# Optimization experiments

Hardware: AMD Instinct MI355X
Metric: run time of the kernel (lower is better)

The kernel has to match this reference:

```python
import jax, jax.numpy as jnp
import numpy as np

EMB = 1024
FF = 1024
EPS = 1e-5

def _layernorm(x, g, b):
    mu = jnp.mean(x, axis=-1, keepdims=True)
    var = jnp.mean((x - mu) ** 2, axis=-1, keepdims=True)
    return (x - mu) * jax.lax.rsqrt(var + EPS) * g + b

def setup_inputs() -> dict:
    key = jax.random.key(0)
    ks = jax.random.split(key, 12)
    s = 1.0 / np.sqrt(EMB)
    x = jax.random.normal(ks[0], (4, 2048, EMB), dtype=jnp.float32)
    Wq = jax.random.normal(ks[1], (EMB, EMB), dtype=jnp.float32) * s
    bq = jnp.zeros((EMB,), jnp.float32)
    Wk = jax.random.normal(ks[2], (EMB, EMB), dtype=jnp.float32) * s
    bk = jnp.zeros((EMB,), jnp.float32)
    Wv = jax.random.normal(ks[3], (EMB, EMB), dtype=jnp.float32) * s
    bv = jnp.zeros((EMB,), jnp.float32)
    Wo = jax.random.normal(ks[4], (EMB, EMB), dtype=jnp.float32) * s
    bo = jnp.zeros((EMB,), jnp.float32)
    W1 = jax.random.normal(ks[5], (EMB, FF), dtype=jnp.float32) * s
    b1 = jnp.zeros((FF,), jnp.float32)
    W2 = jax.random.normal(ks[6], (FF, EMB), dtype=jnp.float32) * (1.0 / np.sqrt(FF))
    b2 = jnp.zeros((EMB,), jnp.float32)
    g1 = jnp.ones((EMB,), jnp.float32); be1 = jnp.zeros((EMB,), jnp.float32)
    g2 = jnp.ones((EMB,), jnp.float32); be2 = jnp.zeros((EMB,), jnp.float32)
    return {"x": x, "Wq": Wq, "bq": bq, "Wk": Wk, "bk": bk, "Wv": Wv, "bv": bv,
            "Wo": Wo, "bo": bo, "W1": W1, "b1": b1, "W2": W2, "b2": b2,
            "g1": g1, "be1": be1, "g2": g2, "be2": be2}

def reference(x, Wq, bq, Wk, bk, Wv, bv, Wo, bo, W1, b1, W2, b2, g1, be1, g2, be2):
    # pre-norm single-head self-attention + residual + FFN (dropout = identity, eval)
    xn = _layernorm(x, g1, be1)
    q = xn @ Wq + bq
    k = xn @ Wk + bk
    v = xn @ Wv + bv
    scores = jnp.einsum('bse,bte->bst', q, k) / jnp.sqrt(jnp.float32(EMB))
    w = jax.nn.softmax(scores, axis=-1)              # [B,S,S]
    attn = jnp.einsum('bst,bte->bse', w, v) @ Wo + bo
    x2 = x + attn
    xn2 = _layernorm(x2, g2, be2)
    ff = jax.nn.relu(xn2 @ W1 + b1) @ W2 + b2
    out = x2 + ff
    return (out, w)
```

## Files before the change

### kernel.cpp

```cpp
#include <hip/hip_runtime.h>

typedef __attribute__((ext_vector_type(8))) __bf16 bf16x8;
typedef __attribute__((ext_vector_type(4))) float f32x4;
typedef __attribute__((ext_vector_type(8))) ushort ushort8;

#define GLP(p) ((const __attribute__((address_space(1))) void*)(p))
#define LDP(p) ((__attribute__((address_space(3))) void*)(p))

__device__ __forceinline__ ushort f2b(float f) {
  union { float f; uint u; } c; c.f = f;
  uint u = c.u;
  uint r = (u + 0x7fffu + ((u >> 16) & 1u)) >> 16;
  return (ushort)r;
}

__device__ __forceinline__ float block_reduce_sum(float v, float* sm) {
#pragma unroll
  for (int off = 1; off < 64; off <<= 1) v += __shfl_xor(v, off);
  const int wave = threadIdx.x >> 6, lane = threadIdx.x & 63;
  __syncthreads();
  if (lane == 0) sm[wave] = v;
  __syncthreads();
  return sm[0] + sm[1] + sm[2] + sm[3];
}

__global__ __launch_bounds__(256) void wtrans6_kernel(
    const float* __restrict__ W0, const float* __restrict__ W1,
    const float* __restrict__ W2, const float* __restrict__ W3,
    const float* __restrict__ W4, const float* __restrict__ W5,
    ushort* __restrict__ T0, ushort* __restrict__ T1, ushort* __restrict__ T2,
    ushort* __restrict__ T3, ushort* __restrict__ T4, ushort* __restrict__ T5) {
  __shared__ float tile[32][33];
  const float* Ws[6] = {W0, W1, W2, W3, W4, W5};
  ushort* Ts[6] = {T0, T1, T2, T3, T4, T5};
  const float* W = Ws[blockIdx.z];
  ushort* Wt = Ts[blockIdx.z];
  const int K = 1024, N = 1024;
  const int n0 = blockIdx.x * 32, k0 = blockIdx.y * 32;
  const int tx = threadIdx.x, ty = threadIdx.y;
#pragma unroll
  for (int i = 0; i < 32; i += 8)
    tile[ty + i][tx] = W[(long)(k0 + ty + i) * N + n0 + tx];
  __syncthreads();
#pragma unroll
  for (int i = 0; i < 32; i += 8)
    Wt[(long)(n0 + ty + i) * K + k0 + tx] = f2b(tile[tx][ty + i]);
}

__global__ __launch_bounds__(256) void layernorm_kernel(
    const float* __restrict__ x, const float* __restrict__ g,
    const float* __restrict__ be, ushort* __restrict__ out) {
  __shared__ float sm[4];
  const long row = blockIdx.x;
  const float4 v = reinterpret_cast<const float4*>(x + row * 1024)[threadIdx.x];
  float s = v.x + v.y + v.z + v.w;
  s = block_reduce_sum(s, sm);
  const float mu = s * (1.0f / 1024.0f);
  const float dx = v.x - mu, dy = v.y - mu, dz = v.z - mu, dw = v.w - mu;
  float s2 = dx * dx + dy * dy + dz * dz + dw * dw;
  s2 = block_reduce_sum(s2, sm);
  const float rstd = rsqrtf(s2 * (1.0f / 1024.0f) + 1e-5f);
  const float4 gg = reinterpret_cast<const float4*>(g)[threadIdx.x];
  const float4 bb = reinterpret_cast<const float4*>(be)[threadIdx.x];
  ushort4 o;
  o.x = f2b(dx * rstd * gg.x + bb.x);
  o.y = f2b(dy * rstd * gg.y + bb.y);
  o.z = f2b(dz * rstd * gg.z + bb.z);
  o.w = f2b(dw * rstd * gg.w + bb.w);
  reinterpret_cast<ushort4*>(out + row * 1024)[threadIdx.x] = o;
}

__global__ __launch_bounds__(256) void softmax_kernel(
    float* __restrict__ s, ushort* __restrict__ wb) {
  __shared__ float sm[4];
  const long row = blockIdx.x;
  float4* r4 = reinterpret_cast<float4*>(s + row * 2048);
  float4 v0 = r4[threadIdx.x * 2];
  float4 v1 = r4[threadIdx.x * 2 + 1];
  float m = fmaxf(fmaxf(fmaxf(v0.x, v0.y), fmaxf(v0.z, v0.w)),
                  fmaxf(fmaxf(v1.x, v1.y), fmaxf(v1.z, v1.w)));
#pragma unroll
  for (int off = 1; off < 64; off <<= 1) m = fmaxf(m, __shfl_xor(m, off));
  const int wave = threadIdx.x >> 6, lane = threadIdx.x & 63;
  if (lane == 0) sm[wave] = m;
  __syncthreads();
  m = fmaxf(fmaxf(sm[0], sm[1]), fmaxf(sm[2], sm[3]));
  v0.x = expf(v0.x - m); v0.y = expf(v0.y - m);
  v0.z = expf(v0.z - m); v0.w = expf(v0.w - m);
  v1.x = expf(v1.x - m); v1.y = expf(v1.y - m);
  v1.z = expf(v1.z - m); v1.w = expf(v1.w - m);
  float sum = v0.x + v0.y + v0.z + v0.w + v1.x + v1.y + v1.z + v1.w;
  sum = block_reduce_sum(sum, sm);
  const float inv = 1.0f / sum;
  v0.x *= inv; v0.y *= inv; v0.z *= inv; v0.w *= inv;
  v1.x *= inv; v1.y *= inv; v1.z *= inv; v1.w *= inv;
  r4[threadIdx.x * 2] = v0;
  r4[threadIdx.x * 2 + 1] = v1;
  ushort8 o;
  o[0] = f2b(v0.x); o[1] = f2b(v0.y); o[2] = f2b(v0.z); o[3] = f2b(v0.w);
  o[4] = f2b(v1.x); o[5] = f2b(v1.y); o[6] = f2b(v1.z); o[7] = f2b(v1.w);
  *reinterpret_cast<ushort8*>(wb + row * 2048 + threadIdx.x * 8) = o;
}

#define EP_BF16 1
#define EP_F32 2
#define EP_BIAS 4
#define EP_RELU 8
#define EP_SCALE 16
#define EP_RESID 32
#define EP_TRANS 64

template <int FLAGS>
__global__ __launch_bounds__(256) void gemm_bt(
    const ushort* __restrict__ A, const ushort* __restrict__ Bt,
    float* __restrict__ Cf, ushort* __restrict__ Cb,
    const float* __restrict__ bias, const float* __restrict__ resid,
    int M, int N, int K, float scale, long sA, long sB, long sC) {
  A += (long)blockIdx.z * sA;
  Bt += (long)blockIdx.z * sB;
  const long coff = (long)blockIdx.z * sC;
  const int tileN = blockIdx.x * 128, tileM = blockIdx.y * 128;
  const int tid = threadIdx.x, lane = tid & 63, wave = tid >> 6;
  const int wm = tid >> 7, wn = (tid >> 6) & 1;
  __shared__ alignas(16) ushort As[2][128][32];
  __shared__ alignas(16) ushort Bs[2][128][32];
  f32x4 acc[4][4] = {};

  const int srow = wave * 32 + (lane >> 2);
  const int scol = (lane & 3) * 8;
  const ushort* aP0 = A + (long)(tileM + srow) * K + scol;
  const ushort* aP1 = aP0 + 16L * K;
  const ushort* bP0 = Bt + (long)(tileN + srow) * K + scol;
  const ushort* bP1 = bP0 + 16L * K;

#define STAGE(buf, kk)                                                                   \
  do {                                                                                   \
    __builtin_amdgcn_global_load_lds(GLP(aP0 + (kk)), LDP(&As[buf][wave * 32][0]), 16,   \
                                     0, 0);                                              \
    __builtin_amdgcn_global_load_lds(GLP(aP1 + (kk)), LDP(&As[buf][wave * 32 + 16][0]),  \
                                     16, 0, 0);                                          \
    __builtin_amdgcn_global_load_lds(GLP(bP0 + (kk)), LDP(&Bs[buf][wave * 32][0]), 16,   \
                                     0, 0);                                              \
    __builtin_amdgcn_global_load_lds(GLP(bP1 + (kk)), LDP(&Bs[buf][wave * 32 + 16][0]),  \
                                     16, 0, 0);                                          \
  } while (0)

  STAGE(0, 0);
  __syncthreads();
  int cur = 0;
  for (int kk = 0; kk < K; kk += 32) {
    const int nxt = cur ^ 1;
    if (kk + 32 < K) STAGE(nxt, kk + 32);
    bf16x8 a[4], b[4];
#pragma unroll
    for (int m = 0; m < 4; ++m)
      a[m] = *reinterpret_cast<const bf16x8*>(
          &As[cur][wm * 64 + m * 16 + (lane & 15)][(lane >> 4) * 8]);
#pragma unroll
    for (int n = 0; n < 4; ++n)
      b[n] = *reinterpret_cast<const bf16x8*>(
          &Bs[cur][wn * 64 + n * 16 + (lane & 15)][(lane >> 4) * 8]);
#pragma unroll
    for (int m = 0; m < 4; ++m)
#pragma unroll
      for (int n = 0; n < 4; ++n)
        acc[m][n] = __builtin_amdgcn_mfma_f32_16x16x32_bf16(a[m], b[n], acc[m][n], 0, 0, 0);
    __syncthreads();
    cur = nxt;
  }
#undef STAGE

  const int row0 = tileM + wm * 64 + ((lane >> 4) << 2);
  const int col0 = tileN + wn * 64 + (lane & 15);
#pragma unroll
  for (int n = 0; n < 4; ++n) {
    const int col = col0 + n * 16;
    const float bv = (FLAGS & EP_BIAS) ? bias[col] : 0.0f;
#pragma unroll
    for (int m = 0; m < 4; ++m) {
#pragma unroll
      for (int i = 0; i < 4; ++i) {
        const int row = row0 + m * 16 + i;
        float v = acc[m][n][i];
        if (FLAGS & EP_SCALE) v *= scale;
        v += bv;
        if (FLAGS & EP_RELU) v = fmaxf(v, 0.0f);
        if (FLAGS & EP_RESID) v += resid[coff + (long)row * N + col];
        if (FLAGS & EP_F32) Cf[coff + (long)row * N + col] = v;
        if (FLAGS & EP_BF16) {
          if (FLAGS & EP_TRANS)
            Cb[coff + (long)col * M + row] = f2b(v);
          else
            Cb[coff + (long)row * N + col] = f2b(v);
        }
      }
    }
  }
}

extern "C" void kernel_launch(void* const* d_in, const int* in_sizes, int n_in,
                              void* d_out, int out_size, void* d_ws, size_t ws_size,
                              hipStream_t stream) {
  const int B = 4, S = 2048, E = 1024, FFD = 1024;
  const long MS = (long)B * S;
  const float* x   = (const float*)d_in[0];
  const float* Wq  = (const float*)d_in[1];
  const float* bq  = (const float*)d_in[2];
  const float* Wk  = (const float*)d_in[3];
  const float* bk  = (const float*)d_in[4];
  const float* Wv  = (const float*)d_in[5];
  const float* bv  = (const float*)d_in[6];
  const float* Wo  = (const float*)d_in[7];
  const float* bo  = (const float*)d_in[8];
  const float* W1  = (const float*)d_in[9];
  const float* b1  = (const float*)d_in[10];
  const float* W2  = (const float*)d_in[11];
  const float* b2  = (const float*)d_in[12];
  const float* g1  = (const float*)d_in[13];
  const float* be1 = (const float*)d_in[14];
  const float* g2  = (const float*)d_in[15];
  const float* be2 = (const float*)d_in[16];

  float* out  = (float*)d_out;
  float* wout = out + MS * E;

  ushort* xnA = (ushort*)d_ws;
  ushort* qB  = xnA + MS * E;
  ushort* kC  = qB + MS * E;
  ushort* vTD = kC + MS * E;
  ushort* wE  = vTD + MS * E;
  float*  x2F = (float*)(wE + (long)B * S * S);
  ushort* wts = (ushort*)(x2F + MS * E);
  ushort* WqT = wts;
  ushort* WkT = WqT + (long)E * E;
  ushort* WvT = WkT + (long)E * E;
  ushort* WoT = WvT + (long)E * E;
  ushort* W1T = WoT + (long)E * E;
  ushort* W2T = W1T + (long)E * FFD;

  hipLaunchKernelGGL(wtrans6_kernel, dim3(E / 32, E / 32, 6), dim3(32, 8), 0, stream,
                     Wq, Wk, Wv, Wo, W1, W2, WqT, WkT, WvT, WoT, W1T, W2T);

  hipLaunchKernelGGL(layernorm_kernel, dim3(MS), dim3(256), 0, stream, x, g1, be1, xnA);

  hipLaunchKernelGGL((gemm_bt<EP_BF16 | EP_BIAS>), dim3(E / 128, MS / 128, 1), dim3(256), 0,
                     stream, xnA, WqT, (float*)nullptr, qB, bq, (const float*)nullptr,
                     (int)MS, E, E, 1.0f, 0L, 0L, 0L);
  hipLaunchKernelGGL((gemm_bt<EP_BF16 | EP_BIAS>), dim3(E / 128, MS / 128, 1), dim3(256), 0,
                     stream, xnA, WkT, (float*)nullptr, kC, bk, (const float*)nullptr,
                     (int)MS, E, E, 1.0f, 0L, 0L, 0L);
  hipLaunchKernelGGL((gemm_bt<EP_BF16 | EP_BIAS | EP_TRANS>), dim3(E / 128, S / 128, B),
                     dim3(256), 0, stream, xnA, WvT, (float*)nullptr, vTD, bv,
                     (const float*)nullptr, S, E, E, 1.0f, (long)S * E, 0L, (long)E * S);

  hipLaunchKernelGGL((gemm_bt<EP_F32 | EP_SCALE>), dim3(S / 128, S / 128, B), dim3(256), 0,
                     stream, qB, kC, wout, (ushort*)nullptr, (const float*)nullptr,
                     (const float*)nullptr, S, S, E, 0.03125f, (long)S * E, (long)S * E,
                     (long)S * S);

  hipLaunchKernelGGL(softmax_kernel, dim3(B * S), dim3(256), 0, stream, wout, wE);

  hipLaunchKernelGGL((gemm_bt<EP_BF16>), dim3(E / 128, S / 128, B), dim3(256), 0, stream,
                     wE, vTD, (float*)nullptr, qB, (const float*)nullptr,
                     (const float*)nullptr, S, E, S, 1.0f, (long)S * S, (long)E * S,
                     (long)S * E);

  hipLaunchKernelGGL((gemm_bt<EP_F32 | EP_BIAS | EP_RESID>), dim3(E / 128, MS / 128, 1),
                     dim3(256), 0, stream, qB, WoT, x2F, (ushort*)nullptr, bo, x,
                     (int)MS, E, E, 1.0f, 0L, 0L, 0L);

  hipLaunchKernelGGL(layernorm_kernel, dim3(MS), dim3(256), 0, stream, x2F, g2, be2, xnA);

  hipLaunchKernelGGL((gemm_bt<EP_BF16 | EP_BIAS | EP_RELU>), dim3(FFD / 128, MS / 128, 1),
                     dim3(256), 0, stream, xnA, W1T, (float*)nullptr, kC, b1,
                     (const float*)nullptr, (int)MS, FFD, E, 1.0f, 0L, 0L, 0L);

  hipLaunchKernelGGL((gemm_bt<EP_F32 | EP_BIAS | EP_RESID>), dim3(E / 128, MS / 128, 1),
                     dim3(256), 0, stream, kC, W2T, out, (ushort*)nullptr, b2, x2F,
                     (int)MS, E, FFD, 1.0f, 0L, 0L, 0L);
}
```

Measured before the change: 362.9 us.

## Add 256x256 pipelined GEMM kernel and fuse QKV projections into one launch

Introduces a 512-thread GEMM with 256x256 output tiles and a 4-slot LDS ring filled by direct global-to-LDS loads, using raw barriers, explicit waitcnt and setprio to overlap loads with MFMA. It is used for a single fused QKV projection, relying on WqT/WkT/WvT being contiguous in memory so they form one 3E-wide weight, and for the Q·K^T score GEMM. This cuts launch count and raises data reuse per tile, at the cost of higher register and LDS pressure (acc[8][4] per thread, 128KB LDS) and the V output being written transposed with strided stores.

```diff
diff --git a/kernel.cpp b/kernel.cpp
--- a/kernel.cpp
+++ b/kernel.cpp
@@ -12,6 +12,16 @@
   uint u = c.u;
   uint r = (u + 0x7fffu + ((u >> 16) & 1u)) >> 16;
   return (ushort)r;
+}
+
+__device__ __forceinline__ void barrier_raw() {
+  asm volatile("" ::: "memory");
+  __builtin_amdgcn_s_barrier();
+  asm volatile("" ::: "memory");
+}
+__device__ __forceinline__ void wait_lgkm0() {
+  asm volatile("s_waitcnt lgkmcnt(0)" ::: "memory");
+  __builtin_amdgcn_sched_barrier(0);
 }
 
 __device__ __forceinline__ float block_reduce_sum(float v, float* sm) {
@@ -192,6 +202,133 @@
             Cb[coff + (long)col * M + row] = f2b(v);
           else
             Cb[coff + (long)row * N + col] = f2b(v);
+        }
+      }
+    }
+  }
+}
+
+template <int MODE>
+__global__ __launch_bounds__(512, 2) void gemm256(
+    const ushort* __restrict__ A, const ushort* __restrict__ Bt,
+    float* __restrict__ Cf,
+    ushort* __restrict__ Cq, ushort* __restrict__ Ck, ushort* __restrict__ Cv,
+    const float* __restrict__ b0, const float* __restrict__ b1,
+    const float* __restrict__ b2,
+    int M, int N, int K, float scale, long sA, long sB, long sC) {
+  A += (long)blockIdx.z * sA;
+  Bt += (long)blockIdx.z * sB;
+  const long coff = (long)blockIdx.z * sC;
+  const int tileN = blockIdx.x * 256, tileM = blockIdx.y * 256;
+  const int tid = threadIdx.x, lane = tid & 63, wid = tid >> 6;
+  const int wr = wid >> 2, wc = wid & 3;
+  __shared__ ushort lds[4][2][8192];
+  f32x4 acc[8][4] = {};
+
+  const int NS = K >> 5;
+
+  const ushort* aSrc = A + (long)(tileM + wid * 32 + (lane >> 2)) * K + (lane & 3) * 8;
+  const ushort* bSrc = Bt + (long)(tileN + wid * 32 + (lane >> 2)) * K + (lane & 3) * 8;
+
+#define STAGE_A256(s)                                                                    \
+  do {                                                                                   \
+    const int sl_ = (s) & 3;                                                             \
+    __builtin_amdgcn_global_load_lds(GLP(aSrc + (long)(s) * 32),                         \
+                                     LDP(&lds[sl_][0][(wid * 2 + 0) * 512]), 16, 0, 0);  \
+    __builtin_amdgcn_global_load_lds(GLP(aSrc + 16L * K + (long)(s) * 32),               \
+                                     LDP(&lds[sl_][0][(wid * 2 + 1) * 512]), 16, 0, 0);  \
+  } while (0)
+#define STAGE_B256(s)                                                                    \
+  do {                                                                                   \
+    const int sl_ = (s) & 3;                                                             \
+    __builtin_amdgcn_global_load_lds(GLP(bSrc + (long)(s) * 32),                         \
+                                     LDP(&lds[sl_][1][(wid * 2 + 0) * 512]), 16, 0, 0);  \
+    __builtin_amdgcn_global_load_lds(GLP(bSrc + 16L * K + (long)(s) * 32),               \
+                                     LDP(&lds[sl_][1][(wid * 2 + 1) * 512]), 16, 0, 0);  \
+  } while (0)
+#define LDA256(sl, f)                                                                    \
+  (*reinterpret_cast<const bf16x8*>(                                                     \
+      &lds[sl][0][(wr * 128 + (f) * 16 + (lane & 15)) * 32 + (lane >> 4) * 8]))
+#define LDB256(sl, f)                                                                    \
+  (*reinterpret_cast<const bf16x8*>(                                                     \
+      &lds[sl][1][(wc * 64 + (f) * 16 + (lane & 15)) * 32 + (lane >> 4) * 8]))
+
+  STAGE_A256(0); STAGE_B256(0);
+  STAGE_A256(1); STAGE_B256(1);
+  STAGE_A256(2); STAGE_B256(2);
+  asm volatile("s_waitcnt vmcnt(8)" ::: "memory");
+  barrier_raw();
+
+  for (int s = 0; s < NS; ++s) {
+    const int sl = s & 3;
+    bf16x8 aF[4], bF[4];
+#pragma unroll
+    for (int f = 0; f < 4; ++f) aF[f] = LDA256(sl, f);
+#pragma unroll
+    for (int f = 0; f < 4; ++f) bF[f] = LDB256(sl, f);
+    if (s + 3 < NS) STAGE_A256(s + 3);
+    barrier_raw();
+    wait_lgkm0();
+    __builtin_amdgcn_s_setprio(1);
+#pragma unroll
+    for (int m = 0; m < 4; ++m)
+#pragma unroll
+      for (int n = 0; n < 4; ++n)
+        acc[m][n] = __builtin_amdgcn_mfma_f32_16x16x32_bf16(aF[m], bF[n], acc[m][n], 0, 0, 0);
+    __builtin_amdgcn_s_setprio(0);
+    barrier_raw();
+#pragma unroll
+    for (int f = 0; f < 4; ++f) aF[f] = LDA256(sl, f + 4);
+    if (s + 3 < NS) STAGE_B256(s + 3);
+    barrier_raw();
+    wait_lgkm0();
+    __builtin_amdgcn_s_setprio(1);
+#pragma unroll
+    for (int m = 0; m < 4; ++m)
+#pragma unroll
+      for (int n = 0; n < 4; ++n)
+        acc[m + 4][n] =
+            __builtin_amdgcn_mfma_f32_16x16x32_bf16(aF[m], bF[n], acc[m + 4][n], 0, 0, 0);
+    __builtin_amdgcn_s_setprio(0);
+    if (s <= NS - 4) {
+      asm volatile("s_waitcnt vmcnt(8)" ::: "memory");
+    } else if (s == NS - 3) {
+      asm volatile("s_waitcnt vmcnt(4)" ::: "memory");
+    } else if (s == NS - 2) {
+      asm volatile("s_waitcnt vmcnt(0)" ::: "memory");
+    }
+    barrier_raw();
+  }
+#undef STAGE_A256
+#undef STAGE_B256
+#undef LDA256
+#undef LDB256
+
+  const int r0 = tileM + wr * 128 + ((lane >> 4) << 2);
+  const int c0 = tileN + wc * 64 + (lane & 15);
+#pragma unroll
+  for (int m = 0; m < 8; ++m) {
+#pragma unroll
+    for (int n = 0; n < 4; ++n) {
+      const int col = c0 + n * 16;
+#pragma unroll
+      for (int i = 0; i < 4; ++i) {
+        const int row = r0 + m * 16 + i;
+        if (MODE == 0) {
+          Cf[coff + (long)row * N + col] = acc[m][n][i] * scale;
+        } else {
+          const int seg = col >> 10, c = col & 1023;
+          const float bias = (seg == 0) ? b0[c] : (seg == 1) ? b1[c] : b2[c];
+          const float v = acc[m][n][i] + bias;
+          if (seg == 0) {
+            Cq[(long)row * 1024 + c] = f2b(v);
+          } else if (seg == 1) {
+            Ck[(long)row * 1024 + c] = f2b(v);
+          } else {
+            const long b = row >> 11;
+            const int s0 = row & 2047;
+            Cv[((b << 10) + c) * 2048 + s0] = f2b(v);
+          }
         }
       }
     }
@@ -243,20 +380,14 @@
 
   hipLaunchKernelGGL(layernorm_kernel, dim3(MS), dim3(256), 0, stream, x, g1, be1, xnA);
 
-  hipLaunchKernelGGL((gemm_bt<EP_BF16 | EP_BIAS>), dim3(E / 128, MS / 128, 1), dim3(256), 0,
-                     stream, xnA, WqT, (float*)nullptr, qB, bq, (const float*)nullptr,
-                     (int)MS, E, E, 1.0f, 0L, 0L, 0L);
-  hipLaunchKernelGGL((gemm_bt<EP_BF16 | EP_BIAS>), dim3(E / 128, MS / 128, 1), dim3(256), 0,
-                     stream, xnA, WkT, (float*)nullptr, kC, bk, (const float*)nullptr,
-                     (int)MS, E, E, 1.0f, 0L, 0L, 0L);
-  hipLaunchKernelGGL((gemm_bt<EP_BF16 | EP_BIAS | EP_TRANS>), dim3(E / 128, S / 128, B),
-                     dim3(256), 0, stream, xnA, WvT, (float*)nullptr, vTD, bv,
-                     (const float*)nullptr, S, E, E, 1.0f, (long)S * E, 0L, (long)E * S);
-
-  hipLaunchKernelGGL((gemm_bt<EP_F32 | EP_SCALE>), dim3(S / 128, S / 128, B), dim3(256), 0,
-                     stream, qB, kC, wout, (ushort*)nullptr, (const float*)nullptr,
-                     (const float*)nullptr, S, S, E, 0.03125f, (long)S * E, (long)S * E,
-                     (long)S * S);
+  hipLaunchKernelGGL((gemm256<1>), dim3(3 * E / 256, MS / 256, 1), dim3(512), 0, stream,
+                     xnA, WqT, (float*)nullptr, qB, kC, vTD, bq, bk, bv,
+                     (int)MS, 3 * E, E, 1.0f, 0L, 0L, 0L);
+
+  hipLaunchKernelGGL((gemm256<0>), dim3(S / 256, S / 256, B), dim3(512), 0, stream,
+                     qB, kC, wout, (ushort*)nullptr, (ushort*)nullptr, (ushort*)nullptr,
+                     (const float*)nullptr, (const float*)nullptr, (const float*)nullptr,
+                     S, S, E, 0.03125f, (long)S * E, (long)S * E, (long)S * S);
 
   hipLaunchKernelGGL(softmax_kernel, dim3(B * S), dim3(256), 0, stream, wout, wE);
 
```

New measurement: 364.3 us. No clear change (+0.4%).
